# Optimization experiments

Measured on AMD Instinct MI355X. Metric: run time of the kernel, lower is better.

Reference implementation:

```python
import jax, jax.numpy as jnp
import numpy as np

PATCH = 14
LEVELS = 6
DIM = 512
MULT = 4
ITERS = 12
TOKEN_ATTEND_SELF_VALUE = -0.0005


def _grouped_ff(x, w1, b1, w2, b2):
    # x: [b, n, g, d]; per-group 1x1 conv == per-level MLP
    h = jnp.einsum('bnld,lmd->bnlm', x, w1) + b1  # [b,n,g,d*mult]
    h = jax.nn.gelu(h, approximate=False)
    return jnp.einsum('bnlm,ldm->bnld', h, w2) + b2


def _consensus(levels):
    # levels: [b, n, l, d]
    d = levels.shape[-1]
    n = levels.shape[1]
    k = levels / jnp.maximum(jnp.linalg.norm(levels, axis=-1, keepdims=True), 1e-12)
    sim = jnp.einsum('bild,bjld->blij', levels, k) * (d ** -0.5)
    self_mask = jnp.eye(n, dtype=bool)[None, None]  # attend_self=False
    sim = jnp.where(self_mask, TOKEN_ATTEND_SELF_VALUE, sim)
    attn = jax.nn.softmax(sim, axis=-1)
    return jnp.einsum('blij,bjld->bild', attn, levels)


def setup_inputs() -> dict:
    key = jax.random.key(0)
    ks = jax.random.split(key, 12)
    b, c, hw = 16, 1, 224
    pd = PATCH * PATCH * c  # 196
    nps = hw // PATCH
    n = nps * nps  # 256
    s = 0.02
    return {
        'img': jax.random.normal(ks[0], (b, c, hw, hw), jnp.float32),
        'to_tokens_w': jax.random.normal(ks[1], (pd, DIM), jnp.float32) * s,
        'to_tokens_b': jnp.zeros((DIM,), jnp.float32),
        'pos_emb': jax.random.normal(ks[2], (n, DIM), jnp.float32) * s,
        'init_levels': jax.random.normal(ks[3], (LEVELS, DIM), jnp.float32),
        'bu_w1': jax.random.normal(ks[4], (LEVELS, DIM * MULT, DIM), jnp.float32) * s,
        'bu_b1': jnp.zeros((LEVELS, DIM * MULT), jnp.float32),
        'bu_w2': jax.random.normal(ks[5], (LEVELS, DIM, DIM * MULT), jnp.float32) * s,
        'bu_b2': jnp.zeros((LEVELS, DIM), jnp.float32),
        'td_w1': jax.random.normal(ks[6], (LEVELS - 1, DIM * MULT, DIM), jnp.float32) * s,
        'td_b1': jnp.zeros((LEVELS - 1, DIM * MULT), jnp.float32),
        'td_w2': jax.random.normal(ks[7], (LEVELS - 1, DIM, DIM * MULT), jnp.float32) * s,
        'td_b2': jnp.zeros((LEVELS - 1, DIM), jnp.float32),
    }


def reference(img, to_tokens_w, to_tokens_b, pos_emb, init_levels,
              bu_w1, bu_b1, bu_w2, bu_b2, td_w1, td_b1, td_w2, td_b2):
    b, c, H, W = img.shape
    hp, wp = H // PATCH, W // PATCH
    n = hp * wp
    # b c (hp p1) (wp p2) -> b (hp wp) (p1 p2 c)
    x = img.reshape(b, c, hp, PATCH, wp, PATCH)
    x = x.transpose(0, 2, 4, 3, 5, 1).reshape(b, n, PATCH * PATCH * c)
    tokens = x @ to_tokens_w + to_tokens_b          # [b, n, d]
    pos = pos_emb[None, :, None, :]                 # [1, n, 1, d]
    bottom = tokens[:, :, None, :]                  # [b, n, 1, d]
    levels0 = jnp.broadcast_to(init_levels[None, None], (b, n, LEVELS, DIM))
    contrib = jnp.array([4., 4., 4., 4., 4., 3.], jnp.float32)[None, None, :, None]

    def step(levels, _):
        lwi = jnp.concatenate((bottom, levels), axis=2)         # [b, n, L+1, d]
        bu = _grouped_ff(lwi[:, :, :-1], bu_w1, bu_b1, bu_w2, bu_b2)
        td = _grouped_ff(lwi[:, :, 2:] + pos, td_w1, td_b1, td_w2, td_b2)
        td = jnp.pad(td, ((0, 0), (0, 0), (0, 1), (0, 0)))      # zero pad top level
        cons = _consensus(levels)
        new_levels = (levels + bu + td + cons) / contrib
        return new_levels, None

    levels, _ = jax.lax.scan(step, levels0, None, length=ITERS)
    return levels
```

## Files before the change

### kernel.cpp

```cpp
#include <hip/hip_runtime.h>
#include <hip/hip_bf16.h>
#include <math.h>

typedef unsigned short ushort_t;

#define DEV __device__ __forceinline__

DEV float bf2f(ushort_t u) {
  return __uint_as_float(((unsigned int)u) << 16);
}
DEV ushort_t f2bf(float f) {
  unsigned int x = __float_as_uint(f);
  return (ushort_t)((x + 0x7FFFu + ((x >> 16) & 1u)) >> 16);
}

DEV float gelu_f(float x) {
  float z = fabsf(x) * 0.70710678118654752f;
  float t = __builtin_amdgcn_rcpf(1.0f + 0.3275911f * z);
  float p = t * (0.254829592f +
            t * (-0.284496736f +
            t * (1.421413741f +
            t * (-1.453152027f +
            t * 1.061405429f))));
  float e = 1.0f - p * __expf(-z * z);
  float s = (x >= 0.f) ? e : -e;
  return 0.5f * x * (1.0f + s);
}

using bf16x8 = __attribute__((ext_vector_type(8))) __bf16;
using f32x4  = __attribute__((ext_vector_type(4))) float;

DEV void gload16(const ushort_t* g, ushort_t* l) {
  __builtin_amdgcn_global_load_lds((const __attribute__((address_space(1))) void*)g,
                                   (__attribute__((address_space(3))) void*)l, 16, 0, 0);
}

DEV void stage_tile(const ushort_t* g, int ld, ushort_t* lds, int t) {
  int w = t >> 6;
#pragma unroll
  for (int r = 0; r < 4; ++r) {
    int chunk = r * 256 + t;
    const ushort_t* gp = g + (size_t)(chunk >> 3) * ld + (size_t)(chunk & 7) * 8;
    ushort_t* lp = lds + (size_t)(r * 256 + w * 64) * 8;
    gload16(gp, lp);
  }
}

DEV void stage_sw(const ushort_t* g, int ld, ushort_t* lds, int t) {
  int w = t >> 6;
#pragma unroll
  for (int r = 0; r < 4; ++r) {
    int chunk = r * 256 + t;
    int row = chunk >> 3;
    int sw  = ((chunk & 7) ^ (row & 7)) * 8;
    const ushort_t* gp = g + (size_t)row * ld + sw;
    ushort_t* lp = lds + (size_t)(r * 256 + w * 64) * 8;
    gload16(gp, lp);
  }
}

template <typename F>
DEV void gemm_tileP(const ushort_t* A, int lda, const ushort_t* B, int ldb, int K, F&& epi) {
  __shared__ alignas(16) ushort_t As[128 * 64];
  __shared__ alignas(16) ushort_t Bs[128 * 64];
  int t = threadIdx.x;
  int lane = t & 63;
  int w = t >> 6;
  int wr = w >> 1, wc = w & 1;
  f32x4 acc[4][4];
#pragma unroll
  for (int m = 0; m < 4; ++m)
#pragma unroll
    for (int n = 0; n < 4; ++n) acc[m][n] = (f32x4){0.f, 0.f, 0.f, 0.f};

  for (int kt = 0; kt < K; kt += 64) {
    __syncthreads();
    stage_tile(A + kt, lda, As, t);
    stage_tile(B + kt, ldb, Bs, t);
    __syncthreads();
#pragma unroll
    for (int kk = 0; kk < 2; ++kk) {
      int kb = kk * 32 + (lane >> 4) * 8;
      bf16x8 af[4], bfr[4];
#pragma unroll
      for (int m = 0; m < 4; ++m)
        af[m] = *(const bf16x8*)&As[(size_t)(wr * 64 + m * 16 + (lane & 15)) * 64 + kb];
#pragma unroll
      for (int n = 0; n < 4; ++n)
        bfr[n] = *(const bf16x8*)&Bs[(size_t)(wc * 64 + n * 16 + (lane & 15)) * 64 + kb];
#pragma unroll
      for (int m = 0; m < 4; ++m)
#pragma unroll
        for (int n = 0; n < 4; ++n)
          acc[m][n] = __builtin_amdgcn_mfma_f32_16x16x32_bf16(af[m], bfr[n], acc[m][n], 0, 0, 0);
    }
  }
  epi(wr, wc, lane, acc);
}

template <typename F>
DEV void gemm_tile(const ushort_t* A, int lda, const ushort_t* B, int ldb, int K, F&& epi) {
  __shared__ alignas(16) ushort_t As[2][128 * 64];
  __shared__ alignas(16) ushort_t Bs[2][128 * 64];
  int t = threadIdx.x;
  int lane = t & 63;
  int w = t >> 6;
  int wr = w >> 1, wc = w & 1;
  const int nk = K >> 6;
  f32x4 acc[4][4];
#pragma unroll
  for (int m = 0; m < 4; ++m)
#pragma unroll
    for (int n = 0; n < 4; ++n) acc[m][n] = (f32x4){0.f, 0.f, 0.f, 0.f};

  int aoff[4][2], boff[4][2];
#pragma unroll
  for (int m = 0; m < 4; ++m)
#pragma unroll
    for (int kk = 0; kk < 2; ++kk) {
      int ks = kk * 4 + (lane >> 4);
      aoff[m][kk] = (wr * 64 + m * 16 + (lane & 15)) * 64 + ((ks ^ (lane & 7)) * 8);
      boff[m][kk] = (wc * 64 + m * 16 + (lane & 15)) * 64 + ((ks ^ (lane & 7)) * 8);
    }

  stage_sw(A, lda, As[0], t);
  stage_sw(B, ldb, Bs[0], t);

  for (int kt = 0; kt < nk; ++kt) {
    int cur = kt & 1;
    int nxt = (kt + 1 < nk) ? kt + 1 : kt;
    stage_sw(A + (size_t)nxt * 64, lda, As[cur ^ 1], t);
    stage_sw(B + (size_t)nxt * 64, ldb, Bs[cur ^ 1], t);
    asm volatile("s_waitcnt vmcnt(8)" ::: "memory");
    __builtin_amdgcn_s_barrier();
    __builtin_amdgcn_sched_barrier(0);
    const ushort_t* asb = &As[cur][0];
    const ushort_t* bsb = &Bs[cur][0];
#pragma unroll
    for (int kk = 0; kk < 2; ++kk) {
      bf16x8 af[4], bfr[4];
#pragma unroll
      for (int m = 0; m < 4; ++m) af[m] = *(const bf16x8*)&asb[aoff[m][kk]];
#pragma unroll
      for (int n = 0; n < 4; ++n) bfr[n] = *(const bf16x8*)&bsb[boff[n][kk]];
      __builtin_amdgcn_s_setprio(1);
#pragma unroll
      for (int m = 0; m < 4; ++m)
#pragma unroll
        for (int n = 0; n < 4; ++n)
          acc[m][n] = __builtin_amdgcn_mfma_f32_16x16x32_bf16(af[m], bfr[n], acc[m][n], 0, 0, 0);
      __builtin_amdgcn_s_setprio(0);
    }
    __builtin_amdgcn_s_barrier();
  }

#pragma unroll
  for (int m = 0; m < 4; ++m)
#pragma unroll
    for (int n = 0; n < 4; ++n)
#pragma unroll
      for (int r = 0; r < 4; ++r) {
        int lr = wr * 64 + m * 16 + (lane >> 4) * 4 + r;
        int lc = wc * 64 + n * 16 + (lane & 15);
        epi(lr, lc, acc[m][n][r]);
      }
}

#define MFMA_QUAD(QM, QN)                                                      \
  _Pragma("unroll") for (int m_ = 0; m_ < 4; ++m_)                             \
  _Pragma("unroll") for (int n_ = 0; n_ < 2; ++n_)                             \
  _Pragma("unroll") for (int kk_ = 0; kk_ < 2; ++kk_)                          \
    acc[QM][QN][m_][n_] = __builtin_amdgcn_mfma_f32_16x16x32_bf16(             \
        aF[m_][kk_], bF[QN][n_][kk_], acc[QM][QN][m_][n_], 0, 0, 0);

template <typename F>
DEV void gemm256(const ushort_t* A, int lda, const ushort_t* B, int ldb, int K, F&& epi) {
  __shared__ alignas(16) ushort_t As[2][256 * 64];
  __shared__ alignas(16) ushort_t Bs[2][256 * 64];
  const int tid = threadIdx.x;
  const int lane = tid & 63;
  const int w = tid >> 6;
  const int ur = w >> 2, uc = w & 3;
  const int nk = K >> 6;

  const int c0 = tid, c1 = 512 + tid;
  const int row0 = c0 >> 3, row1 = c1 >> 3;
  const int sw0 = ((c0 & 7) ^ (row0 & 7)) * 8;
  const int sw1 = ((c1 & 7) ^ (row1 & 7)) * 8;
  const ushort_t* Ab0 = A + (size_t)row0 * lda + sw0;
  const ushort_t* Ab1 = A + (size_t)row1 * lda + sw1;
  const ushort_t* Bb0 = B + (size_t)row0 * ldb + sw0;
  const ushort_t* Bb1 = B + (size_t)row1 * ldb + sw1;
  const int ld0 = (0 * 512 + w * 64) * 8;
  const int ld1 = (1 * 512 + w * 64) * 8;

  auto stageA = [&](int t, int hh, int b) {
    const ushort_t* g0 = Ab0 + (size_t)hh * 128 * lda + t * 64;
    const ushort_t* g1 = Ab1 + (size_t)hh * 128 * lda + t * 64;
    ushort_t* l = &As[b][hh * 8192];
    gload16(g0, l + ld0);
    gload16(g1, l + ld1);
  };
  auto stageB = [&](int t, int hh, int b) {
    const ushort_t* g0 = Bb0 + (size_t)hh * 128 * ldb + t * 64;
    const ushort_t* g1 = Bb1 + (size_t)hh * 128 * ldb + t * 64;
    ushort_t* l = &Bs[b][hh * 8192];
    gload16(g0, l + ld0);
    gload16(g1, l + ld1);
  };

  int aoff[4][2], boff[2][2];
#pragma unroll
  for (int m = 0; m < 4; ++m)
#pragma unroll
    for (int kk = 0; kk < 2; ++kk) {
      int row = ur * 64 + m * 16 + (lane & 15);
      int ks = kk * 4 + (lane >> 4);
      aoff[m][kk] = row * 64 + ((ks ^ (lane & 7)) * 8);
    }
#pragma unroll
  for (int n = 0; n < 2; ++n)
#pragma unroll
    for (int kk = 0; kk < 2; ++kk) {
      int row = uc * 32 + n * 16 + (lane & 15);
      int ks = kk * 4 + (lane >> 4);
      boff[n][kk] = row * 64 + ((ks ^ (lane & 7)) * 8);
    }

  f32x4 acc[2][2][4][2];
#pragma unroll
  for (int qm = 0; qm < 2; ++qm)
#pragma unroll
    for (int qn = 0; qn < 2; ++qn)
#pragma unroll
      for (int m = 0; m < 4; ++m)
#pragma unroll
        for (int n = 0; n < 2; ++n) acc[qm][qn][m][n] = (f32x4){0.f, 0.f, 0.f, 0.f};

  stageA(0, 0, 0);
  stageB(0, 0, 0);
  stageB(0, 1, 0);
  stageA(0, 1, 0);
  stageA(1, 0, 1);
  stageB(1, 0, 1);
  asm volatile("s_waitcnt vmcnt(8)" ::: "memory");
  __builtin_amdgcn_s_barrier();

  bf16x8 aF[4][2], bF[2][2][2];

  for (int t = 0; t < nk; ++t) {
    const int b = t & 1;
    const ushort_t* asb = &As[b][0];
    const ushort_t* bsb = &Bs[b][0];
    const int t1 = (t + 1 < nk) ? t + 1 : nk - 1;
    const int t2 = (t + 2 < nk) ? t + 2 : nk - 1;

#pragma unroll
    for (int m = 0; m < 4; ++m)
#pragma unroll
      for (int kk = 0; kk < 2; ++kk) aF[m][kk] = *(const bf16x8*)&asb[aoff[m][kk]];
#pragma unroll
    for (int n = 0; n < 2; ++n)
#pragma unroll
      for (int kk = 0; kk < 2; ++kk) bF[0][n][kk] = *(const bf16x8*)&bsb[boff[n][kk]];
    stageB(t1, 1, (t + 1) & 1);
    __builtin_amdgcn_s_barrier();
    asm volatile("s_waitcnt lgkmcnt(0)" ::: "memory");
    __builtin_amdgcn_s_setprio(1);
    MFMA_QUAD(0, 0)
    __builtin_amdgcn_s_setprio(0);
    asm volatile("s_waitcnt vmcnt(8)" ::: "memory");
    __builtin_amdgcn_s_barrier();

#pragma unroll
    for (int n = 0; n < 2; ++n)
#pragma unroll
      for (int kk = 0; kk < 2; ++kk) bF[1][n][kk] = *(const bf16x8*)&bsb[boff[n][kk] + 8192];
    stageA(t1, 1, (t + 1) & 1);
    __builtin_amdgcn_s_barrier();
    asm volatile("s_waitcnt lgkmcnt(0)" ::: "memory");
    __builtin_amdgcn_s_setprio(1);
    MFMA_QUAD(0, 1)
    __builtin_amdgcn_s_setprio(0);
    asm volatile("s_waitcnt vmcnt(8)" ::: "memory");
    __builtin_amdgcn_s_barrier();

#pragma unroll
    for (int m = 0; m < 4; ++m)
#pragma unroll
      for (int kk = 0; kk < 2; ++kk) aF[m][kk] = *(const bf16x8*)&asb[aoff[m][kk] + 8192];
    stageA(t2, 0, b);
    __builtin_amdgcn_s_barrier();
    asm volatile("s_waitcnt lgkmcnt(0)" ::: "memory");
    __builtin_amdgcn_s_setprio(1);
    MFMA_QUAD(1, 0)
    __builtin_amdgcn_s_setprio(0);
    __builtin_amdgcn_s_barrier();

    stageB(t2, 0, b);
    __builtin_amdgcn_s_barrier();
    __builtin_amdgcn_s_setprio(1);
    MFMA_QUAD(1, 1)
    __builtin_amdgcn_s_setprio(0);
    asm volatile("s_waitcnt vmcnt(8)" ::: "memory");
    __builtin_amdgcn_s_barrier();
  }
  asm volatile("s_waitcnt vmcnt(0)" ::: "memory");

#pragma unroll
  for (int qm = 0; qm < 2; ++qm)
#pragma unroll
    for (int qn = 0; qn < 2; ++qn)
#pragma unroll
      for (int m = 0; m < 4; ++m)
#pragma unroll
        for (int n = 0; n < 2; ++n)
#pragma unroll
          for (int r = 0; r < 4; ++r) {
            int lr = qm * 128 + ur * 64 + m * 16 + (lane >> 4) * 4 + r;
            int lc = qn * 128 + uc * 32 + n * 16 + (lane & 15);
            epi(lr, lc, acc[qm][qn][m][n][r]);
          }
}

__global__ __launch_bounds__(256) void ff1_kernel(
    int g0, const ushort_t* tokens, const ushort_t* levels_bf, const ushort_t* levels_pos,
    const ushort_t* w1_bf, const float* bu_b1, const float* td_b1, ushort_t* h) {
  int g = g0 + blockIdx.z;
  int tm = blockIdx.x, tn = blockIdx.y;
  const ushort_t* A; int lda;
  if (g == 0)      { A = tokens     + (size_t)tm * 128 * 512;                              lda = 512;  }
  else if (g < 6)  { A = levels_bf  + (size_t)tm * 128 * 3072 + (size_t)(g - 1) * 512;     lda = 3072; }
  else             { A = levels_pos + (size_t)tm * 128 * 2560 + (size_t)(g - 6) * 512;     lda = 2560; }
  const ushort_t* W = w1_bf + (size_t)g * 2048 * 512 + (size_t)tn * 128 * 512;
  const float* bias = (g < 6) ? (bu_b1 + (size_t)g * 2048) : (td_b1 + (size_t)(g - 6) * 2048);
  ushort_t* out = h + ((size_t)(g - g0) * 4096 + (size_t)tm * 128) * 2048 + (size_t)tn * 128;
  gemm_tileP(A, lda, W, 512, 512, [&](int wr, int wc, int lane, f32x4 (&acc)[4][4]) {
#pragma unroll
    for (int m = 0; m < 4; ++m)
#pragma unroll
      for (int q = 0; q < 2; ++q) {
        int col = wc * 64 + q * 32 + 2 * (lane & 15);
        float b0 = bias[tn * 128 + col];
        float b1 = bias[tn * 128 + col + 1];
#pragma unroll
        for (int r = 0; r < 4; ++r) {
          int lr = wr * 64 + m * 16 + (lane >> 4) * 4 + r;
          float x0 = gelu_f(acc[m][2 * q][r] + b0);
          float x1 = gelu_f(acc[m][2 * q + 1][r] + b1);
          unsigned int pk = (unsigned int)f2bf(x0) | ((unsigned int)f2bf(x1) << 16);
          *(unsigned int*)&out[(size_t)lr * 2048 + col] = pk;
        }
      }
  });
}

__global__ __launch_bounds__(512, 2) void ff2_kernel(
    int g0, const ushort_t* h, const ushort_t* w2_bf, const float* bu_b2, const float* td_b2,
    float* levels) {
  int g = g0 + blockIdx.z;
  int tm = blockIdx.x, tn = blockIdx.y;
  const ushort_t* A = h + ((size_t)(g - g0) * 4096 + (size_t)tm * 256) * 2048;
  const ushort_t* W = w2_bf + (size_t)g * 512 * 2048 + (size_t)tn * 256 * 2048;
  int l = (g < 6) ? g : (g - 6);
  const float* bias = (g < 6) ? (bu_b2 + (size_t)g * 512) : (td_b2 + (size_t)(g - 6) * 512);
  gemm256(A, 2048, W, 2048, 2048, [&](int lr, int lc, float v) {
    int bn = tm * 256 + lr;
    int d  = tn * 256 + lc;
    size_t idx = ((size_t)bn * 6 + l) * 512 + d;
    levels[idx] += v + bias[d];
  });
}

__global__ __launch_bounds__(256) void sim_kernel(const ushort_t* levels_bf, const float* invn,
                                                  ushort_t* simattn) {
  int bl = blockIdx.z; int tm = blockIdx.x, tn = blockIdx.y;
  int b = bl / 6, l = bl % 6;
  const ushort_t* A = levels_bf + ((size_t)(b * 256 + tm * 128) * 6 + l) * 512;
  const ushort_t* B = levels_bf + ((size_t)(b * 256 + tn * 128) * 6 + l) * 512;
  const float* inv = invn + (size_t)bl * 256;
  ushort_t* out = simattn + ((size_t)bl * 256 + tm * 128) * 256 + (size_t)tn * 128;
  gemm_tile(A, 3072, B, 3072, 512, [&](int lr, int lc, float v) {
    int i = tm * 128 + lr, j = tn * 128 + lc;
    float s = (i == j) ? -0.0005f : v * inv[j] * 0.044194173824159216f;
    out[(size_t)lr * 256 + lc] = f2bf(s);
  });
}

__global__ __launch_bounds__(256) void softmax_kernel(ushort_t* simattn) {
  int row = blockIdx.x, t = threadIdx.x;
  __shared__ float red[256];
  float x = bf2f(simattn[(size_t)row * 256 + t]);
  red[t] = x;
  __syncthreads();
  for (int s = 128; s > 0; s >>= 1) { if (t < s) red[t] = fmaxf(red[t], red[t + s]); __syncthreads(); }
  float mx = red[0];
  __syncthreads();
  float e = __expf(x - mx);
  red[t] = e;
  __syncthreads();
  for (int s = 128; s > 0; s >>= 1) { if (t < s) red[t] += red[t + s]; __syncthreads(); }
  float den = red[0];
  simattn[(size_t)row * 256 + t] = f2bf(e / den);
}

__global__ __launch_bounds__(256) void pv_kernel(const ushort_t* attn, const ushort_t* levelsT,
                                                 float* levels) {
  int bl = blockIdx.z; int tm = blockIdx.x, tn = blockIdx.y;
  int b = bl / 6, l = bl % 6;
  const ushort_t* A = attn + (size_t)bl * 256 * 256 + (size_t)tm * 128 * 256;
  const ushort_t* B = levelsT + ((size_t)bl * 512 + (size_t)tn * 128) * 256;
  gemm_tile(A, 256, B, 256, 256, [&](int lr, int lc, float v) {
    int n = tm * 128 + lr;
    int d = tn * 128 + lc;
    size_t idx = (((size_t)b * 256 + n) * 6 + l) * 512 + d;
    levels[idx] += v;
  });
}

__global__ __launch_bounds__(128) void prep_kernel(float* levels, const float* pos_emb,
                                                   ushort_t* levels_bf, ushort_t* levels_pos,
                                                   float* invn, int apply) {
  int bid = blockIdx.x;
  int l = bid % 6;
  int bn = bid / 6;
  int n = bn & 255, b = bn >> 8;
  int t = threadIdx.x;
  float4 lv = *(const float4*)&levels[(size_t)bid * 512 + t * 4];
  if (apply) {
    float rc = (l == 5) ? (1.0f / 3.0f) : 0.25f;
    lv.x *= rc; lv.y *= rc; lv.z *= rc; lv.w *= rc;
    *(float4*)&levels[(size_t)bid * 512 + t * 4] = lv;
  }
  float ss = lv.x * lv.x + lv.y * lv.y + lv.z * lv.z + lv.w * lv.w;
#pragma unroll
  for (int off = 32; off > 0; off >>= 1) ss += __shfl_down(ss, off);
  __shared__ float s2[2];
  if ((t & 63) == 0) s2[t >> 6] = ss;
  __syncthreads();
  if (t == 0) {
    float tot = s2[0] + s2[1];
    invn[(size_t)(b * 6 + l) * 256 + n] = 1.0f / fmaxf(sqrtf(tot), 1e-12f);
  }
  ushort4 o;
  o.x = f2bf(lv.x); o.y = f2bf(lv.y); o.z = f2bf(lv.z); o.w = f2bf(lv.w);
  *(ushort4*)&levels_bf[(size_t)bid * 512 + t * 4] = o;
  if (l >= 1) {
    float4 pu = *(const float4*)&pos_emb[(size_t)n * 512 + t * 4];
    ushort4 op;
    op.x = f2bf(lv.x + pu.x);
    op.y = f2bf(lv.y + pu.y);
    op.z = f2bf(lv.z + pu.z);
    op.w = f2bf(lv.w + pu.w);
    *(ushort4*)&levels_pos[((size_t)bn * 5 + (l - 1)) * 512 + t * 4] = op;
  }
}

__global__ __launch_bounds__(256) void transpose_kernel(const float* levels, ushort_t* levelsT) {
  int bl = blockIdx.z; int b = bl / 6, l = bl % 6;
  int n0 = blockIdx.y * 64, d0 = blockIdx.x * 64;
  __shared__ ushort_t tile[64][72];
  int t = threadIdx.x;
#pragma unroll
  for (int rr = 0; rr < 2; ++rr) {
    int c = t + rr * 256;
    int r = c >> 3, c8 = (c & 7) * 8;
    const float* src = &levels[(((size_t)(b * 256 + n0 + r)) * 6 + l) * 512 + d0 + c8];
    float4 v0 = *(const float4*)src;
    float4 v1 = *(const float4*)(src + 4);
    tile[r][c8 + 0] = f2bf(v0.x); tile[r][c8 + 1] = f2bf(v0.y);
    tile[r][c8 + 2] = f2bf(v0.z); tile[r][c8 + 3] = f2bf(v0.w);
    tile[r][c8 + 4] = f2bf(v1.x); tile[r][c8 + 5] = f2bf(v1.y);
    tile[r][c8 + 6] = f2bf(v1.z); tile[r][c8 + 7] = f2bf(v1.w);
  }
  __syncthreads();
#pragma unroll
  for (int rr = 0; rr < 2; ++rr) {
    int c = t + rr * 256;
    int dr = c >> 3, n8 = (c & 7) * 8;
    ushort4 o0, o1;
    o0.x = tile[n8 + 0][dr]; o0.y = tile[n8 + 1][dr]; o0.z = tile[n8 + 2][dr]; o0.w = tile[n8 + 3][dr];
    o1.x = tile[n8 + 4][dr]; o1.y = tile[n8 + 5][dr]; o1.z = tile[n8 + 6][dr]; o1.w = tile[n8 + 7][dr];
    ushort_t* dst = &levelsT[((size_t)bl * 512 + d0 + dr) * 256 + n0 + n8];
    *(ushort4*)dst = o0;
    *(ushort4*)(dst + 4) = o1;
  }
}

__global__ __launch_bounds__(256) void tokens_kernel(const float* img, const float* ttw,
                                                     const float* ttb, ushort_t* tokens) {
  int token = blockIdx.x;
  int b = token >> 8, n = token & 255;
  int ph = n >> 4, pw = n & 15;
  __shared__ float patch[196];
  int t = threadIdx.x;
  if (t < 196) {
    int r = t / 14, cc = t % 14;
    patch[t] = img[(size_t)b * 50176 + (size_t)(ph * 14 + r) * 224 + pw * 14 + cc];
  }
  __syncthreads();
  float a0 = ttb[t];
  float a1 = ttb[t + 256];
  for (int k = 0; k < 196; ++k) {
    float p = patch[k];
    a0 += p * ttw[(size_t)k * 512 + t];
    a1 += p * ttw[(size_t)k * 512 + t + 256];
  }
  tokens[(size_t)token * 512 + t]       = f2bf(a0);
  tokens[(size_t)token * 512 + t + 256] = f2bf(a1);
}

__global__ void init_kernel(const float* init_levels, float* levels) {
  size_t i4 = (size_t)blockIdx.x * 256 + threadIdx.x;
  size_t e0 = i4 * 4;
  int idx = (int)(e0 % 3072);
  *(float4*)&levels[e0] = *(const float4*)&init_levels[idx];
}

__global__ void scale_kernel(float* levels) {
  size_t i4 = (size_t)blockIdx.x * 256 + threadIdx.x;
  size_t e0 = i4 * 4;
  int l = (int)((e0 >> 9) % 6);
  float rc = (l == 5) ? (1.0f / 3.0f) : 0.25f;
  float4 a = *(const float4*)&levels[e0];
  float4 o = {a.x * rc, a.y * rc, a.z * rc, a.w * rc};
  *(float4*)&levels[e0] = o;
}

__global__ void cvt_kernel(const float* src, ushort_t* dst, int n4) {
  int i = blockIdx.x * 256 + threadIdx.x;
  if (i >= n4) return;
  float4 v = ((const float4*)src)[i];
  ushort4 o;
  o.x = f2bf(v.x); o.y = f2bf(v.y); o.z = f2bf(v.z); o.w = f2bf(v.w);
  ((ushort4*)dst)[i] = o;
}

__global__ void cvt_w1_kernel(const float* src, ushort_t* dst, int nrows) {
  int i = blockIdx.x * 256 + threadIdx.x;
  if (i >= nrows * 128) return;
  int row = i >> 7, k4 = (i & 127) * 4;
  int grp = row >> 11, rr = row & 2047;
  int p = (rr & ~31) | ((rr & 1) << 4) | ((rr & 31) >> 1);
  float4 v = *(const float4*)&src[(size_t)row * 512 + k4];
  ushort4 o;
  o.x = f2bf(v.x); o.y = f2bf(v.y); o.z = f2bf(v.z); o.w = f2bf(v.w);
  *(ushort4*)&dst[((size_t)(grp << 11) + p) * 512 + k4] = o;
}

extern "C" void kernel_launch(void* const* d_in, const int* in_sizes, int n_in,
                              void* d_out, int out_size, void* d_ws, size_t ws_size,
                              hipStream_t stream) {
  const float* img    = (const float*)d_in[0];
  const float* ttw    = (const float*)d_in[1];
  const float* ttb    = (const float*)d_in[2];
  const float* pos    = (const float*)d_in[3];
  const float* initlv = (const float*)d_in[4];
  const float* bu_w1  = (const float*)d_in[5];
  const float* bu_b1  = (const float*)d_in[6];
  const float* bu_w2  = (const float*)d_in[7];
  const float* bu_b2  = (const float*)d_in[8];
  const float* td_w1  = (const float*)d_in[9];
  const float* td_b1  = (const float*)d_in[10];
  const float* td_w2  = (const float*)d_in[11];
  const float* td_b2  = (const float*)d_in[12];

  float* levels = (float*)d_out;

  const size_t HB = 16777216ull;

  char* p = (char*)d_ws;
  auto alloc = [&](size_t bytes) { char* r = p; p += (bytes + 255) & ~(size_t)255; return r; };
  float*    invn       = (float*)alloc(24576ull * 4);
  ushort_t* tokens     = (ushort_t*)alloc(2097152ull * 2);
  ushort_t* levels_bf  = (ushort_t*)alloc(12582912ull * 2);
  ushort_t* levels_pos = (ushort_t*)alloc(10485760ull * 2);
  ushort_t* levelsT    = (ushort_t*)alloc(12582912ull * 2);
  ushort_t* simattn    = (ushort_t*)alloc(6291456ull * 2);
  ushort_t* w1_bf      = (ushort_t*)alloc(11534336ull * 2);
  ushort_t* w2_bf      = (ushort_t*)alloc(11534336ull * 2);
  size_t used = (size_t)(p - (char*)d_ws);
  if (used + HB > ws_size) return;
  int gpp = (int)((ws_size - used) / HB);
  if (gpp > 6) gpp = 6;
  ushort_t* h = (ushort_t*)alloc((size_t)gpp * HB);

  cvt_w1_kernel<<<6144, 256, 0, stream>>>(bu_w1, w1_bf, 12288);
  cvt_w1_kernel<<<5120, 256, 0, stream>>>(td_w1, w1_bf + 6291456ull, 10240);
  cvt_kernel<<<6144, 256, 0, stream>>>(bu_w2, w2_bf, 1572864);
  cvt_kernel<<<5120, 256, 0, stream>>>(td_w2, w2_bf + 6291456ull, 1310720);
  tokens_kernel<<<4096, 256, 0, stream>>>(img, ttw, ttb, tokens);
  init_kernel<<<12288, 256, 0, stream>>>(initlv, levels);

  for (int it = 0; it < 12; ++it) {
    prep_kernel<<<24576, 128, 0, stream>>>(levels, pos, levels_bf, levels_pos, invn,
                                           it > 0 ? 1 : 0);
    transpose_kernel<<<dim3(8, 4, 96), 256, 0, stream>>>(levels, levelsT);
    sim_kernel<<<dim3(2, 2, 96), 256, 0, stream>>>(levels_bf, invn, simattn);
    softmax_kernel<<<24576, 256, 0, stream>>>(simattn);
    pv_kernel<<<dim3(2, 4, 96), 256, 0, stream>>>(simattn, levelsT, levels);
    for (int g0 = 0; g0 < 11; g0 += gpp) {
      int gn = 11 - g0 < gpp ? 11 - g0 : gpp;
      ff1_kernel<<<dim3(32, 16, gn), 256, 0, stream>>>(g0, tokens, levels_bf, levels_pos,
                                                       w1_bf, bu_b1, td_b1, h);
      ff2_kernel<<<dim3(16, 2, gn), 512, 0, stream>>>(g0, h, w2_bf, bu_b2, td_b2, levels);
    }
  }
  scale_kernel<<<12288, 256, 0, stream>>>(levels);
}
```

Measured before the change: 5.383 ms.

## Register-prefetch swizzled GEMM tiles in ff1 and use wave-per-row softmax

The ff1 GEMM now loads the next K tile into registers while MFMAs run on the current one. It writes tiles to LDS with an XOR swizzle to avoid bank conflicts and raises wave priority around the MFMA block. This hides global-load latency that the previous direct-to-LDS, unpipelined tile path exposed. Separately, softmax now handles one 256-wide row per wavefront using shuffle reductions and 4-element vector loads, which removes the LDS tree reductions and many barriers and cuts the block count by four. The extra prefetch registers may lower occupancy.

After: 10.52 ms. +95.5%, slower.

```diff
diff --git a/kernel.cpp b/kernel.cpp
--- a/kernel.cpp
+++ b/kernel.cpp
@@ -29,21 +29,11 @@
 
 using bf16x8 = __attribute__((ext_vector_type(8))) __bf16;
 using f32x4  = __attribute__((ext_vector_type(4))) float;
+struct u32x4 { unsigned int x, y, z, w; };
 
 DEV void gload16(const ushort_t* g, ushort_t* l) {
   __builtin_amdgcn_global_load_lds((const __attribute__((address_space(1))) void*)g,
                                    (__attribute__((address_space(3))) void*)l, 16, 0, 0);
-}
-
-DEV void stage_tile(const ushort_t* g, int ld, ushort_t* lds, int t) {
-  int w = t >> 6;
-#pragma unroll
-  for (int r = 0; r < 4; ++r) {
-    int chunk = r * 256 + t;
-    const ushort_t* gp = g + (size_t)(chunk >> 3) * ld + (size_t)(chunk & 7) * 8;
-    ushort_t* lp = lds + (size_t)(r * 256 + w * 64) * 8;
-    gload16(gp, lp);
-  }
 }
 
 DEV void stage_sw(const ushort_t* g, int ld, ushort_t* lds, int t) {
@@ -60,39 +50,77 @@
 }
 
 template <typename F>
-DEV void gemm_tileP(const ushort_t* A, int lda, const ushort_t* B, int ldb, int K, F&& epi) {
+DEV void gemm_tileR(const ushort_t* A, int lda, const ushort_t* B, int ldb, int K, F&& epi) {
   __shared__ alignas(16) ushort_t As[128 * 64];
   __shared__ alignas(16) ushort_t Bs[128 * 64];
   int t = threadIdx.x;
   int lane = t & 63;
   int w = t >> 6;
   int wr = w >> 1, wc = w & 1;
+  const int nk = K >> 6;
   f32x4 acc[4][4];
 #pragma unroll
   for (int m = 0; m < 4; ++m)
 #pragma unroll
     for (int n = 0; n < 4; ++n) acc[m][n] = (f32x4){0.f, 0.f, 0.f, 0.f};
 
-  for (int kt = 0; kt < K; kt += 64) {
-    __syncthreads();
-    stage_tile(A + kt, lda, As, t);
-    stage_tile(B + kt, ldb, Bs, t);
-    __syncthreads();
+  int aoff[4][2], boff[4][2];
+#pragma unroll
+  for (int m = 0; m < 4; ++m)
 #pragma unroll
     for (int kk = 0; kk < 2; ++kk) {
-      int kb = kk * 32 + (lane >> 4) * 8;
+      int ks = kk * 4 + (lane >> 4);
+      aoff[m][kk] = (wr * 64 + m * 16 + (lane & 15)) * 64 + ((ks ^ (lane & 7)) * 8);
+      boff[m][kk] = (wc * 64 + m * 16 + (lane & 15)) * 64 + ((ks ^ (lane & 7)) * 8);
+    }
+
+  u32x4 ra[4], rb[4];
+  auto loadreg = [&](const ushort_t* g, int ld, u32x4* rr) {
+#pragma unroll
+    for (int r = 0; r < 4; ++r) {
+      int chunk = r * 256 + t;
+      rr[r] = *(const u32x4*)&g[(size_t)(chunk >> 3) * ld + (size_t)(chunk & 7) * 8];
+    }
+  };
+  auto writelds = [&](ushort_t* lds, u32x4* rr) {
+#pragma unroll
+    for (int r = 0; r < 4; ++r) {
+      int chunk = r * 256 + t;
+      int row = chunk >> 3;
+      int sl  = (chunk & 7) ^ (row & 7);
+      *(u32x4*)&lds[(size_t)(row * 8 + sl) * 8] = rr[r];
+    }
+  };
+
+  loadreg(A, lda, ra);
+  loadreg(B, ldb, rb);
+
+  for (int kt = 0; kt < nk; ++kt) {
+    asm volatile("s_waitcnt vmcnt(0)" ::: "memory");
+    __builtin_amdgcn_s_barrier();
+    writelds(As, ra);
+    writelds(Bs, rb);
+    __builtin_amdgcn_s_barrier();
+    asm volatile("s_waitcnt lgkmcnt(0)" ::: "memory");
+    __builtin_amdgcn_sched_barrier(0);
+    if (kt + 1 < nk) {
+      loadreg(A + (size_t)(kt + 1) * 64, lda, ra);
+      loadreg(B + (size_t)(kt + 1) * 64, ldb, rb);
+    }
+#pragma unroll
+    for (int kk = 0; kk < 2; ++kk) {
       bf16x8 af[4], bfr[4];
 #pragma unroll
-      for (int m = 0; m < 4; ++m)
-        af[m] = *(const bf16x8*)&As[(size_t)(wr * 64 + m * 16 + (lane & 15)) * 64 + kb];
-#pragma unroll
-      for (int n = 0; n < 4; ++n)
-        bfr[n] = *(const bf16x8*)&Bs[(size_t)(wc * 64 + n * 16 + (lane & 15)) * 64 + kb];
+      for (int m = 0; m < 4; ++m) af[m] = *(const bf16x8*)&As[aoff[m][kk]];
+#pragma unroll
+      for (int n = 0; n < 4; ++n) bfr[n] = *(const bf16x8*)&Bs[boff[n][kk]];
+      __builtin_amdgcn_s_setprio(1);
 #pragma unroll
       for (int m = 0; m < 4; ++m)
 #pragma unroll
         for (int n = 0; n < 4; ++n)
           acc[m][n] = __builtin_amdgcn_mfma_f32_16x16x32_bf16(af[m], bfr[n], acc[m][n], 0, 0, 0);
+      __builtin_amdgcn_s_setprio(0);
     }
   }
   epi(wr, wc, lane, acc);
@@ -335,7 +363,7 @@
   const ushort_t* W = w1_bf + (size_t)g * 2048 * 512 + (size_t)tn * 128 * 512;
   const float* bias = (g < 6) ? (bu_b1 + (size_t)g * 2048) : (td_b1 + (size_t)(g - 6) * 2048);
   ushort_t* out = h + ((size_t)(g - g0) * 4096 + (size_t)tm * 128) * 2048 + (size_t)tn * 128;
-  gemm_tileP(A, lda, W, 512, 512, [&](int wr, int wc, int lane, f32x4 (&acc)[4][4]) {
+  gemm_tileR(A, lda, W, 512, 512, [&](int wr, int wc, int lane, f32x4 (&acc)[4][4]) {
 #pragma unroll
     for (int m = 0; m < 4; ++m)
 #pragma unroll
@@ -388,20 +416,21 @@
 }
 
 __global__ __launch_bounds__(256) void softmax_kernel(ushort_t* simattn) {
-  int row = blockIdx.x, t = threadIdx.x;
-  __shared__ float red[256];
-  float x = bf2f(simattn[(size_t)row * 256 + t]);
-  red[t] = x;
-  __syncthreads();
-  for (int s = 128; s > 0; s >>= 1) { if (t < s) red[t] = fmaxf(red[t], red[t + s]); __syncthreads(); }
-  float mx = red[0];
-  __syncthreads();
-  float e = __expf(x - mx);
-  red[t] = e;
-  __syncthreads();
-  for (int s = 128; s > 0; s >>= 1) { if (t < s) red[t] += red[t + s]; __syncthreads(); }
-  float den = red[0];
-  simattn[(size_t)row * 256 + t] = f2bf(e / den);
+  int row = blockIdx.x * 4 + (threadIdx.x >> 6);
+  int lane = threadIdx.x & 63;
+  ushort_t* p = simattn + (size_t)row * 256 + lane * 4;
+  ushort4 u = *(const ushort4*)p;
+  float x0 = bf2f(u.x), x1 = bf2f(u.y), x2 = bf2f(u.z), x3 = bf2f(u.w);
+  float mx = fmaxf(fmaxf(x0, x1), fmaxf(x2, x3));
+#pragma unroll
+  for (int off = 32; off > 0; off >>= 1) mx = fmaxf(mx, __shfl_xor(mx, off));
+  float e0 = __expf(x0 - mx), e1 = __expf(x1 - mx), e2 = __expf(x2 - mx), e3 = __expf(x3 - mx);
+  float s = e0 + e1 + e2 + e3;
+#pragma unroll
+  for (int off = 32; off > 0; off >>= 1) s += __shfl_xor(s, off);
+  float r = __builtin_amdgcn_rcpf(s);
+  u.x = f2bf(e0 * r); u.y = f2bf(e1 * r); u.z = f2bf(e2 * r); u.w = f2bf(e3 * r);
+  *(ushort4*)p = u;
 }
 
 __global__ __launch_bounds__(256) void pv_kernel(const ushort_t* attn, const ushort_t* levelsT,
@@ -597,7 +626,7 @@
                                            it > 0 ? 1 : 0);
     transpose_kernel<<<dim3(8, 4, 96), 256, 0, stream>>>(levels, levelsT);
     sim_kernel<<<dim3(2, 2, 96), 256, 0, stream>>>(levels_bf, invn, simattn);
-    softmax_kernel<<<24576, 256, 0, stream>>>(simattn);
+    softmax_kernel<<<6144, 256, 0, stream>>>(simattn);
     pv_kernel<<<dim3(2, 4, 96), 256, 0, stream>>>(simattn, levelsT, levels);
     for (int g0 = 0; g0 < 11; g0 += gpp) {
       int gn = 11 - g0 < gpp ? 11 - g0 : gpp;
```
